# Optimization experiments

Hardware: AMD Instinct MI355X
Metric: run time of the kernel (lower is better)

The kernel has to match this reference:

```python
import jax, jax.numpy as jnp
import numpy as np

EPS = 1e-5
S = 4        # s_scale
K = 3        # adjacency subsets
CB = 32      # per-branch channels


def _bn(x, g, b, m, v):
    # inference-mode BatchNorm2d over channel axis 1 of [n,c,t,v]
    scale = g * jax.lax.rsqrt(v + EPS)
    shift = b - m * scale
    return x * scale[None, :, None, None] + shift[None, :, None, None]


def _conv1x1(x, w, b):
    # pointwise conv: x [n,c,t,v], w [o,c], b [o]
    return jnp.einsum('nctv,oc->notv', x, w) + b[None, :, None, None]


def setup_inputs() -> dict:
    key = jax.random.key(0)
    ks = jax.random.split(key, 24)
    d = {}
    d['x'] = jax.random.normal(ks[0], (64, 256, 64, 25), jnp.float32)
    d['A'] = jax.random.uniform(ks[1], (K, 25, 25), jnp.float32)
    d['reduct_w'] = jax.random.normal(ks[2], (128, 256), jnp.float32) * 0.05
    d['reduct_b'] = jax.random.normal(ks[3], (128,), jnp.float32) * 0.05
    d['rg'] = jax.random.uniform(ks[4], (128,), jnp.float32) + 0.5
    d['rb'] = jax.random.normal(ks[5], (128,), jnp.float32) * 0.05
    d['rm'] = jax.random.normal(ks[6], (128,), jnp.float32) * 0.05
    d['rv'] = jax.random.uniform(ks[7], (128,), jnp.float32) + 0.5
    d['gcn_w'] = jax.random.normal(ks[8], (S, K * CB, CB), jnp.float32) * 0.1
    d['gcn_b'] = jax.random.normal(ks[9], (S, K * CB), jnp.float32) * 0.05
    d['PA'] = jax.random.normal(ks[10], (S, K, 25, 25), jnp.float32) * 0.05
    d['bg'] = jax.random.uniform(ks[11], (S, CB), jnp.float32) + 0.5
    d['bb'] = jax.random.normal(ks[12], (S, CB), jnp.float32) * 0.05
    d['bm'] = jax.random.normal(ks[13], (S, CB), jnp.float32) * 0.05
    d['bv'] = jax.random.uniform(ks[14], (S, CB), jnp.float32) + 0.5
    d['exp_w'] = jax.random.normal(ks[15], (256, 128), jnp.float32) * 0.05
    d['exp_b'] = jax.random.normal(ks[16], (256,), jnp.float32) * 0.05
    d['eg'] = jax.random.uniform(ks[17], (256,), jnp.float32) + 0.5
    d['eb'] = jax.random.normal(ks[18], (256,), jnp.float32) * 0.05
    d['em'] = jax.random.normal(ks[19], (256,), jnp.float32) * 0.05
    d['ev'] = jax.random.uniform(ks[20], (256,), jnp.float32) + 0.5
    return d


def reference(x, A, reduct_w, reduct_b, rg, rb, rm, rv, gcn_w, gcn_b, PA,
              bg, bb, bm, bv, exp_w, exp_b, eg, eb, em, ev):
    res = x  # identity residual (in_channels == out_channels)
    h = jax.nn.relu(_bn(_conv1x1(x, reduct_w, reduct_b), rg, rb, rm, rv))
    n, c, t, v = h.shape
    spx = jnp.split(h, S, axis=1)  # S chunks of CB channels
    outs = []
    sp = None
    for i in range(S):  # res2net sequential accumulation ('basic' mode)
        sp = spx[i] if i == 0 else sp + spx[i]
        g = _conv1x1(sp, gcn_w[i], gcn_b[i])           # [n, K*CB, t, v]
        g = g.reshape(n, K, CB, t, v)
        g = jnp.einsum('nkctv,kvw->nctw', g, A + PA[i])
        sp = jax.nn.relu(_bn(g, bg[i], bb[i], bm[i], bv[i]))
        outs.append(sp)
    h = jnp.concatenate(outs, axis=1)                  # [n, 4*CB, t, v]
    out = jax.nn.relu(_bn(_conv1x1(h, exp_w, exp_b), eg, eb, em, ev) + res)
    return out
```

## Files before the change

kernel.cpp:

```cpp
#include <hip/hip_runtime.h>
#include <cstdint>
#include <cstddef>

#define EPSV 1e-5f

using f32x4  = __attribute__((ext_vector_type(4))) float;
using bf16x8 = __attribute__((ext_vector_type(8))) short;

static __device__ __forceinline__ unsigned pk2(float lo, float hi) {
    unsigned a = __builtin_bit_cast(unsigned, lo);
    unsigned b = __builtin_bit_cast(unsigned, hi);
    a = (a + 0x7FFFu + ((a >> 16) & 1u)) >> 16;
    b = (b + 0x7FFFu + ((b >> 16) & 1u)) & 0xFFFF0000u;
    return a | b;
}
static __device__ __forceinline__ unsigned short bf16of(float v) {
    return (unsigned short)(pk2(v, 0.f) & 0xFFFFu);
}
static __device__ __forceinline__ float f32of(unsigned short u) {
    return __builtin_bit_cast(float, (unsigned)u << 16);
}
static __device__ __forceinline__ void unpk2(unsigned u, float& lo, float& hi) {
    lo = __builtin_bit_cast(float, u << 16);
    hi = __builtin_bit_cast(float, u & 0xFFFF0000u);
}

__global__ __launch_bounds__(256) void prep_params(
    const float* __restrict__ rwb, const float* __restrict__ rg,
    const float* __restrict__ rb,  const float* __restrict__ rm,
    const float* __restrict__ rv,
    const float* __restrict__ ewb, const float* __restrict__ eg,
    const float* __restrict__ eb,  const float* __restrict__ em,
    const float* __restrict__ ev,
    const float* __restrict__ bg,  const float* __restrict__ bb,
    const float* __restrict__ bm,  const float* __restrict__ bv,
    float* __restrict__ prm)
{
    int t = threadIdx.x;
    if (t < 128) {
        float sc = rg[t] * rsqrtf(rv[t] + EPSV);
        prm[t]       = sc;
        prm[128 + t] = rb[t] - rm[t] * sc + rwb[t] * sc;
        float bsc = bg[t] * rsqrtf(bv[t] + EPSV);
        prm[768 + t] = bsc;
        prm[896 + t] = bb[t] - bm[t] * bsc;
    }
    {
        float sc = eg[t] * rsqrtf(ev[t] + EPSV);
        prm[256 + t] = sc;
        prm[512 + t] = eb[t] - em[t] * sc + ewb[t] * sc;
    }
}

#define LDR 40

template<int BMODE, int OUTMODE>
__global__ __launch_bounds__(256) void gemm_v3(
    const void* __restrict__ Bsrc,
    const float* __restrict__ Wt,
    const float* __restrict__ scale,
    const float* __restrict__ shift,
    const float* __restrict__ resid,
    void* __restrict__ OutP,
    int Cin, int O, int P)
{
    const int n    = blockIdx.z;
    const int p0   = blockIdx.x * 64;
    const int o0   = blockIdx.y * 128;
    const int tid  = threadIdx.x;
    const int lane = tid & 63;
    const int wid  = tid >> 6;
    const int wm   = wid >> 1, wn = wid & 1;
    const int rl   = lane & 15;

    constexpr int SMEM = (BMODE == 0)
        ? (20480 + 16384)
        : ((20480 + 10240) < 32768 ? 32768 : (20480 + 10240));
    __shared__ __align__(16) char smem[SMEM];
    short* sA = (short*)smem;

    const int ao = tid >> 1;
    const int ak = (tid & 1) * 16;

    f32x4 acc[4][2];
    #pragma unroll
    for (int i = 0; i < 4; ++i)
        #pragma unroll
        for (int j = 0; j < 2; ++j) acc[i][j] = (f32x4)0.f;

    float4 ra[4];
    float4 rb0, rb1;
    uint4  rbu;

    const int nt = Cin >> 5;

    auto load_regs = [&](int t) {
        const int kc = t << 5;
        const float* wrow = Wt + (size_t)(o0 + ao) * Cin + kc + ak;
        #pragma unroll
        for (int i = 0; i < 4; ++i)
            ra[i] = *(const float4*)(wrow + i * 4);
        if constexpr (BMODE == 0) {
            const float* bp = (const float*)Bsrc + (size_t)n * Cin * P;
            int s0 = tid, s1 = tid + 256;
            rb0 = *(const float4*)(bp + (size_t)(kc + (s0 >> 4)) * P + p0 + ((s0 & 15) << 2));
            rb1 = *(const float4*)(bp + (size_t)(kc + (s1 >> 4)) * P + p0 + ((s1 & 15) << 2));
        } else {
            const unsigned short* bp = (const unsigned short*)Bsrc;
            int p = tid >> 2, k8 = (tid & 3) << 3;
            rbu = *(const uint4*)(bp + ((size_t)n * P + p0 + p) * Cin + kc + k8);
        }
    };

    auto write_lds = [&](int buf) {
        short* a = sA + buf * (128 * LDR);
        uint4 w0 = make_uint4(pk2(ra[0].x, ra[0].y), pk2(ra[0].z, ra[0].w),
                              pk2(ra[1].x, ra[1].y), pk2(ra[1].z, ra[1].w));
        uint4 w1 = make_uint4(pk2(ra[2].x, ra[2].y), pk2(ra[2].z, ra[2].w),
                              pk2(ra[3].x, ra[3].y), pk2(ra[3].z, ra[3].w));
        *(uint4*)(a + ao * LDR + ak)     = w0;
        *(uint4*)(a + ao * LDR + ak + 8) = w1;
        if constexpr (BMODE == 0) {
            float* sBf = (float*)(smem + 20480) + buf * 2048;
            int s0 = tid, s1 = tid + 256;
            int k0r = s0 >> 4, p40 = (s0 & 15) << 2;
            int k1r = s1 >> 4, p41 = (s1 & 15) << 2;
            *(float4*)(&sBf[(k0r << 6) + ((p40 + (((k0r >> 3) & 7) << 3)) & 63)]) = rb0;
            *(float4*)(&sBf[(k1r << 6) + ((p41 + (((k1r >> 3) & 7) << 3)) & 63)]) = rb1;
        } else {
            short* sB = (short*)(smem + 20480) + buf * (64 * LDR);
            int p = tid >> 2, k8 = (tid & 3) << 3;
            *(uint4*)(sB + p * LDR + k8) = rbu;
        }
    };

    auto compute = [&](int buf) {
        const short* a = sA + buf * (128 * LDR);
        const int k0 = (lane >> 4) * 8;
        bf16x8 af[4], bfr[2];
        #pragma unroll
        for (int i = 0; i < 4; ++i)
            af[i] = *(const bf16x8*)(a + (wm * 64 + i * 16 + rl) * LDR + k0);
        if constexpr (BMODE == 0) {
            const float* sBf = (const float*)(smem + 20480) + buf * 2048;
            #pragma unroll
            for (int j = 0; j < 2; ++j) {
                int p = wn * 32 + j * 16 + rl;
                int base = (p + ((k0 >> 3) << 3)) & 63;
                float f[8];
                #pragma unroll
                for (int q = 0; q < 8; ++q)
                    f[q] = sBf[((k0 + q) << 6) + base];
                uint4 u = make_uint4(pk2(f[0], f[1]), pk2(f[2], f[3]),
                                     pk2(f[4], f[5]), pk2(f[6], f[7]));
                bfr[j] = __builtin_bit_cast(bf16x8, u);
            }
        } else {
            const short* sB = (const short*)(smem + 20480) + buf * (64 * LDR);
            #pragma unroll
            for (int j = 0; j < 2; ++j)
                bfr[j] = *(const bf16x8*)(sB + (wn * 32 + j * 16 + rl) * LDR + k0);
        }
        #pragma unroll
        for (int i = 0; i < 4; ++i)
            #pragma unroll
            for (int j = 0; j < 2; ++j)
                acc[i][j] = __builtin_amdgcn_mfma_f32_16x16x32_bf16(
                    af[i], bfr[j], acc[i][j], 0, 0, 0);
    };

    load_regs(0);
    write_lds(0);
    for (int t = 0; t < nt; ++t) {
        if (t + 1 < nt) load_regs(t + 1);
        __syncthreads();
        compute(t & 1);
        if (t + 1 < nt) write_lds((t + 1) & 1);
    }

    if constexpr (OUTMODE == 1) {
        __syncthreads();
        unsigned short* eL = (unsigned short*)smem;
        #pragma unroll
        for (int i = 0; i < 4; ++i) {
            #pragma unroll
            for (int r = 0; r < 4; ++r) {
                int ol = wm * 64 + i * 16 + (lane >> 4) * 4 + r;
                int o  = o0 + ol;
                float sc = scale[o], sh = shift[o];
                #pragma unroll
                for (int j = 0; j < 2; ++j) {
                    int p = wn * 32 + j * 16 + rl;
                    float v = fmaxf(fmaf(acc[i][j][r], sc, sh), 0.f);
                    eL[p * 128 + (ol ^ ((p & 15) << 3))] = bf16of(v);
                }
            }
        }
        __syncthreads();
        unsigned short* out = (unsigned short*)OutP;
        #pragma unroll
        for (int it = 0; it < 4; ++it) {
            int idx = tid + it * 256;
            int p = idx >> 4, m = idx & 15;
            uint4 u = *(const uint4*)(&eL[p * 128 + ((m ^ (p & 15)) << 3)]);
            *(uint4*)(out + ((size_t)n * P + p0 + p) * O + (m << 3)) = u;
        }
    } else {
        __syncthreads();
        float* eT = (float*)smem;
        #pragma unroll
        for (int i = 0; i < 4; ++i) {
            #pragma unroll
            for (int r = 0; r < 4; ++r) {
                int ol = wm * 64 + i * 16 + (lane >> 4) * 4 + r;
                int o  = o0 + ol;
                float sc = scale[o], sh = shift[o];
                #pragma unroll
                for (int j = 0; j < 2; ++j) {
                    int p = wn * 32 + j * 16 + rl;
                    eT[(ol << 6) + ((p + ((ol & 7) << 3)) & 63)] =
                        fmaf(acc[i][j][r], sc, sh);
                }
            }
        }
        __syncthreads();
        float* out = (float*)OutP;
        #pragma unroll
        for (int it = 0; it < 8; ++it) {
            int idx = tid + it * 256;
            int ol = idx >> 4, p4 = (idx & 15) << 2;
            float4 v = *(const float4*)(&eT[(ol << 6) + ((p4 + ((ol & 7) << 3)) & 63)]);
            size_t base = ((size_t)n * O + o0 + ol) * P + p0 + p4;
            if (resid) {
                float4 r4 = *(const float4*)(resid + base);
                v.x += r4.x; v.y += r4.y; v.z += r4.z; v.w += r4.w;
            }
            v.x = fmaxf(v.x, 0.f); v.y = fmaxf(v.y, 0.f);
            v.z = fmaxf(v.z, 0.f); v.w = fmaxf(v.w, 0.f);
            *(float4*)(out + base) = v;
        }
    }
}

__global__ __launch_bounds__(256) void gcn_fused(
    const unsigned short* __restrict__ hT,
    unsigned short* __restrict__ outsT,
    const float* __restrict__ gw,
    const float* __restrict__ gb,
    const float* __restrict__ Aadj,
    const float* __restrict__ PA,
    const float* __restrict__ bsc4,
    const float* __restrict__ bsh4)
{
    const int n  = blockIdx.y;
    const int tt = blockIdx.x;
    const int tid = threadIdx.x;
    const int c  = tid & 31;
    const int tl = tid >> 5;

    __shared__ unsigned short spb[200 * 32];
    __shared__ float wsg[96 * 33];
    __shared__ float Mm[3][25][28];
    __shared__ unsigned short outb[200 * 32];

    const size_t rowbase = (size_t)n * 1600 + (size_t)tt * 200;

    {
        const unsigned short* hrow = hT + rowbase * 128;
        for (int idx = tid; idx < 800; idx += 256) {
            int p = idx >> 2, c8 = (idx & 3) << 3;
            *(uint4*)(&spb[p * 32 + c8]) =
                *(const uint4*)(hrow + (size_t)p * 128 + c8);
        }
        for (int idx = tid; idx < 96 * 32; idx += 256)
            wsg[(idx >> 5) * 33 + (idx & 31)] = gw[idx];
        for (int idx = tid; idx < 1875; idx += 256) {
            int k = idx / 625, rem = idx % 625;
            Mm[k][rem / 25][rem % 25] = Aadj[idx] + PA[idx];
        }
    }
    __syncthreads();

    for (int step = 0; step < 4; ++step) {
        float g[3][25];
        {
            const float* gbp = gb + step * 96;
            float b0 = gbp[c], b1 = gbp[32 + c], b2 = gbp[64 + c];
            #pragma unroll
            for (int v = 0; v < 25; ++v) { g[0][v] = b0; g[1][v] = b1; g[2][v] = b2; }
        }
        const unsigned short* srow = spb + tl * 25 * 32;
        for (int cin = 0; cin < 32; ++cin) {
            float w0 = wsg[c * 33 + cin];
            float w1 = wsg[(32 + c) * 33 + cin];
            float w2 = wsg[(64 + c) * 33 + cin];
            #pragma unroll
            for (int v = 0; v < 25; ++v) {
                float sv = f32of(srow[v * 32 + cin]);
                g[0][v] = fmaf(w0, sv, g[0][v]);
                g[1][v] = fmaf(w1, sv, g[1][v]);
                g[2][v] = fmaf(w2, sv, g[2][v]);
            }
        }

        float out[25];
        #pragma unroll
        for (int w = 0; w < 25; ++w) out[w] = 0.f;
        #pragma unroll
        for (int k = 0; k < 3; ++k)
            #pragma unroll
            for (int v = 0; v < 25; ++v) {
                float gv = g[k][v];
                #pragma unroll
                for (int w = 0; w < 25; ++w)
                    out[w] = fmaf(gv, Mm[k][v][w], out[w]);
            }

        {
            float sc = bsc4[step * 32 + c], sh = bsh4[step * 32 + c];
            #pragma unroll
            for (int w = 0; w < 25; ++w)
                out[w] = fmaxf(fmaf(out[w], sc, sh), 0.f);
        }

        __syncthreads();

        #pragma unroll
        for (int w = 0; w < 25; ++w) {
            unsigned short b = bf16of(out[w]);
            spb[(tl * 25 + w) * 32 + c]  = b;
            outb[(tl * 25 + w) * 32 + c] = b;
        }
        __syncthreads();

        {
            unsigned short* orow = outsT + rowbase * 128 + step * 32;
            for (int idx = tid; idx < 800; idx += 256) {
                int p = idx >> 2, c8 = (idx & 3) << 3;
                uint4 u = *(const uint4*)(&outb[p * 32 + c8]);
                *(uint4*)(orow + (size_t)p * 128 + c8) = u;
            }
        }

        if (step < 3) {
            const unsigned short* hrow = hT + rowbase * 128 + (step + 1) * 32;
            for (int idx = tid; idx < 800; idx += 256) {
                int p = idx >> 2, c8 = (idx & 3) << 3;
                uint4 u = *(const uint4*)(hrow + (size_t)p * 128 + c8);
                uint4 s = *(const uint4*)(&spb[p * 32 + c8]);
                float hf[8], sf[8];
                unpk2(u.x, hf[0], hf[1]); unpk2(u.y, hf[2], hf[3]);
                unpk2(u.z, hf[4], hf[5]); unpk2(u.w, hf[6], hf[7]);
                unpk2(s.x, sf[0], sf[1]); unpk2(s.y, sf[2], sf[3]);
                unpk2(s.z, sf[4], sf[5]); unpk2(s.w, sf[6], sf[7]);
                uint4 r = make_uint4(pk2(sf[0] + hf[0], sf[1] + hf[1]),
                                     pk2(sf[2] + hf[2], sf[3] + hf[3]),
                                     pk2(sf[4] + hf[4], sf[5] + hf[5]),
                                     pk2(sf[6] + hf[6], sf[7] + hf[7]));
                *(uint4*)(&spb[p * 32 + c8]) = r;
            }
            const float* gwp = gw + (step + 1) * 96 * 32;
            for (int idx = tid; idx < 96 * 32; idx += 256)
                wsg[(idx >> 5) * 33 + (idx & 31)] = gwp[idx];
            const float* pap = PA + (step + 1) * 1875;
            for (int idx = tid; idx < 1875; idx += 256) {
                int k = idx / 625, rem = idx % 625;
                Mm[k][rem / 25][rem % 25] = Aadj[idx] + pap[idx];
            }
            __syncthreads();
        }
    }
}

extern "C" void kernel_launch(void* const* d_in, const int* in_sizes, int n_in,
                              void* d_out, int out_size, void* d_ws, size_t ws_size,
                              hipStream_t stream)
{
    const float* x   = (const float*)d_in[0];
    const float* A   = (const float*)d_in[1];
    const float* rw  = (const float*)d_in[2];
    const float* rwb = (const float*)d_in[3];
    const float* rg  = (const float*)d_in[4];
    const float* rb  = (const float*)d_in[5];
    const float* rm  = (const float*)d_in[6];
    const float* rv  = (const float*)d_in[7];
    const float* gw  = (const float*)d_in[8];
    const float* gb  = (const float*)d_in[9];
    const float* PA  = (const float*)d_in[10];
    const float* bg  = (const float*)d_in[11];
    const float* bb  = (const float*)d_in[12];
    const float* bm  = (const float*)d_in[13];
    const float* bv  = (const float*)d_in[14];
    const float* ew  = (const float*)d_in[15];
    const float* ewb = (const float*)d_in[16];
    const float* eg  = (const float*)d_in[17];
    const float* eb  = (const float*)d_in[18];
    const float* em  = (const float*)d_in[19];
    const float* ev  = (const float*)d_in[20];

    char* wsb = (char*)d_ws;
    unsigned short* hT    = (unsigned short*)wsb;
    unsigned short* outsT = (unsigned short*)(wsb + 26214400);
    float*          prm   = (float*)(wsb + 52428800);

    prep_params<<<1, 256, 0, stream>>>(rwb, rg, rb, rm, rv,
                                       ewb, eg, eb, em, ev,
                                       bg, bb, bm, bv, prm);

    gemm_v3<0, 1><<<dim3(25, 1, 64), 256, 0, stream>>>(
        x, rw, prm, prm + 128, nullptr, hT, 256, 128, 1600);

    gcn_fused<<<dim3(8, 64), 256, 0, stream>>>(
        hT, outsT, gw, gb, A, PA, prm + 768, prm + 896);

    gemm_v3<1, 0><<<dim3(25, 2, 64), 256, 0, stream>>>(
        outsT, ew, prm + 256, prm + 512, x, d_out, 128, 256, 1600);
}
```

Baseline: 194.6 us.

## Split GCN vertex work across two half-waves and combine with cross-lane shuffle

The fused GCN kernel now launches 512 threads per block instead of 256. Each (time, channel) pair is split across two half-wavefronts, one handling vertices 0-12 and the other 13-24. Each half computes a partial adjacency product over all 25 output vertices, and the halves are summed with a lane-xor-32 shuffle. This halves per-thread register arrays and doubles available parallelism to lift occupancy and latency hiding, at the cost of a 13/12 imbalance and extra shuffle traffic.

```diff
diff --git a/kernel.cpp b/kernel.cpp
--- a/kernel.cpp
+++ b/kernel.cpp
@@ -242,7 +242,7 @@
     }
 }
 
-__global__ __launch_bounds__(256) void gcn_fused(
+__global__ __launch_bounds__(512) void gcn_fused(
     const unsigned short* __restrict__ hT,
     unsigned short* __restrict__ outsT,
     const float* __restrict__ gw,
@@ -256,7 +256,10 @@
     const int tt = blockIdx.x;
     const int tid = threadIdx.x;
     const int c  = tid & 31;
-    const int tl = tid >> 5;
+    const int h  = (tid >> 5) & 1;
+    const int t  = tid >> 6;
+    const int v0 = h * 13;
+    const int nv = 13 - h;
 
     __shared__ unsigned short spb[200 * 32];
     __shared__ float wsg[96 * 33];
@@ -267,14 +270,14 @@
 
     {
         const unsigned short* hrow = hT + rowbase * 128;
-        for (int idx = tid; idx < 800; idx += 256) {
+        for (int idx = tid; idx < 800; idx += 512) {
             int p = idx >> 2, c8 = (idx & 3) << 3;
             *(uint4*)(&spb[p * 32 + c8]) =
                 *(const uint4*)(hrow + (size_t)p * 128 + c8);
         }
-        for (int idx = tid; idx < 96 * 32; idx += 256)
+        for (int idx = tid; idx < 96 * 32; idx += 512)
             wsg[(idx >> 5) * 33 + (idx & 31)] = gw[idx];
-        for (int idx = tid; idx < 1875; idx += 256) {
+        for (int idx = tid; idx < 1875; idx += 512) {
             int k = idx / 625, rem = idx % 625;
             Mm[k][rem / 25][rem % 25] = Aadj[idx] + PA[idx];
         }
@@ -282,60 +285,70 @@
     __syncthreads();
 
     for (int step = 0; step < 4; ++step) {
-        float g[3][25];
+        float g[3][13];
         {
             const float* gbp = gb + step * 96;
             float b0 = gbp[c], b1 = gbp[32 + c], b2 = gbp[64 + c];
             #pragma unroll
-            for (int v = 0; v < 25; ++v) { g[0][v] = b0; g[1][v] = b1; g[2][v] = b2; }
-        }
-        const unsigned short* srow = spb + tl * 25 * 32;
+            for (int v = 0; v < 13; ++v) { g[0][v] = b0; g[1][v] = b1; g[2][v] = b2; }
+        }
+        const unsigned short* srow = spb + (t * 25 + v0) * 32;
         for (int cin = 0; cin < 32; ++cin) {
             float w0 = wsg[c * 33 + cin];
             float w1 = wsg[(32 + c) * 33 + cin];
             float w2 = wsg[(64 + c) * 33 + cin];
             #pragma unroll
-            for (int v = 0; v < 25; ++v) {
-                float sv = f32of(srow[v * 32 + cin]);
-                g[0][v] = fmaf(w0, sv, g[0][v]);
-                g[1][v] = fmaf(w1, sv, g[1][v]);
-                g[2][v] = fmaf(w2, sv, g[2][v]);
-            }
-        }
-
-        float out[25];
-        #pragma unroll
-        for (int w = 0; w < 25; ++w) out[w] = 0.f;
+            for (int v = 0; v < 13; ++v) {
+                if (v < nv) {
+                    float sv = f32of(srow[v * 32 + cin]);
+                    g[0][v] = fmaf(w0, sv, g[0][v]);
+                    g[1][v] = fmaf(w1, sv, g[1][v]);
+                    g[2][v] = fmaf(w2, sv, g[2][v]);
+                }
+            }
+        }
+
+        float part[25];
+        #pragma unroll
+        for (int w = 0; w < 25; ++w) part[w] = 0.f;
         #pragma unroll
         for (int k = 0; k < 3; ++k)
             #pragma unroll
-            for (int v = 0; v < 25; ++v) {
-                float gv = g[k][v];
-                #pragma unroll
-                for (int w = 0; w < 25; ++w)
-                    out[w] = fmaf(gv, Mm[k][v][w], out[w]);
-            }
-
-        {
-            float sc = bsc4[step * 32 + c], sh = bsh4[step * 32 + c];
-            #pragma unroll
-            for (int w = 0; w < 25; ++w)
-                out[w] = fmaxf(fmaf(out[w], sc, sh), 0.f);
-        }
-
-        __syncthreads();
-
-        #pragma unroll
-        for (int w = 0; w < 25; ++w) {
-            unsigned short b = bf16of(out[w]);
-            spb[(tl * 25 + w) * 32 + c]  = b;
-            outb[(tl * 25 + w) * 32 + c] = b;
+            for (int v = 0; v < 13; ++v) {
+                if (v < nv) {
+                    float gv = g[k][v];
+                    #pragma unroll
+                    for (int w = 0; w < 25; ++w)
+                        part[w] = fmaf(gv, Mm[k][v0 + v][w], part[w]);
+                }
+            }
+
+        float out[13];
+        float sc = bsc4[step * 32 + c], sh = bsh4[step * 32 + c];
+        #pragma unroll
+        for (int wg = 0; wg < 25; ++wg) {
+            float full = part[wg] + __shfl_xor(part[wg], 32);
+            int w = wg - v0;
+            if (w >= 0 && w < nv)
+                out[w] = fmaxf(fmaf(full, sc, sh), 0.f);
+        }
+
+        __syncthreads();
+
+        #pragma unroll
+        for (int w = 0; w < 13; ++w) {
+            if (w < nv) {
+                unsigned short b = bf16of(out[w]);
+                int p = t * 25 + v0 + w;
+                spb[p * 32 + c]  = b;
+                outb[p * 32 + c] = b;
+            }
         }
         __syncthreads();
 
         {
             unsigned short* orow = outsT + rowbase * 128 + step * 32;
-            for (int idx = tid; idx < 800; idx += 256) {
+            for (int idx = tid; idx < 800; idx += 512) {
                 int p = idx >> 2, c8 = (idx & 3) << 3;
                 uint4 u = *(const uint4*)(&outb[p * 32 + c8]);
                 *(uint4*)(orow + (size_t)p * 128 + c8) = u;
@@ -344,7 +357,7 @@
 
         if (step < 3) {
             const unsigned short* hrow = hT + rowbase * 128 + (step + 1) * 32;
-            for (int idx = tid; idx < 800; idx += 256) {
+            for (int idx = tid; idx < 800; idx += 512) {
                 int p = idx >> 2, c8 = (idx & 3) << 3;
                 uint4 u = *(const uint4*)(hrow + (size_t)p * 128 + c8);
                 uint4 s = *(const uint4*)(&spb[p * 32 + c8]);
@@ -360,10 +373,10 @@
                 *(uint4*)(&spb[p * 32 + c8]) = r;
             }
             const float* gwp = gw + (step + 1) * 96 * 32;
-            for (int idx = tid; idx < 96 * 32; idx += 256)
+            for (int idx = tid; idx < 96 * 32; idx += 512)
                 wsg[(idx >> 5) * 33 + (idx & 31)] = gwp[idx];
             const float* pap = PA + (step + 1) * 1875;
-            for (int idx = tid; idx < 1875; idx += 256) {
+            for (int idx = tid; idx < 1875; idx += 512) {
                 int k = idx / 625, rem = idx % 625;
                 Mm[k][rem / 25][rem % 25] = Aadj[idx] + pap[idx];
             }
@@ -410,7 +423,7 @@
     gemm_v3<0, 1><<<dim3(25, 1, 64), 256, 0, stream>>>(
         x, rw, prm, prm + 128, nullptr, hT, 256, 128, 1600);
 
-    gcn_fused<<<dim3(8, 64), 256, 0, stream>>>(
+    gcn_fused<<<dim3(8, 64), 512, 0, stream>>>(
         hT, outsT, gw, gb, A, PA, prm + 768, prm + 896);
 
     gemm_v3<1, 0><<<dim3(25, 2, 64), 256, 0, stream>>>(
```

After: 239.9 us. 23.3% more time.
